# Kernel optimization log

Hardware: AMD Instinct MI355X
Metric: run time of the kernel (lower is better)

The kernel has to match this reference:

```python
import jax, jax.numpy as jnp
import numpy as np

B, T, D, H = 2, 2048, 1024, 16
HD = D // H  # head_dim = 64


def setup_inputs() -> dict:
    key = jax.random.key(0)
    ks = jax.random.split(key, 5)
    s = 0.02
    return {
        "x": jax.random.normal(ks[0], (B, T, D), dtype=jnp.float32),
        "Wqkv": jax.random.normal(ks[1], (3 * D, D), dtype=jnp.float32) * s,
        "bqkv": jax.random.normal(ks[2], (3 * D,), dtype=jnp.float32) * s,
        "Wproj": jax.random.normal(ks[3], (D, D), dtype=jnp.float32) * s,
        "bproj": jax.random.normal(ks[4], (D,), dtype=jnp.float32) * s,
    }


def reference(x, Wqkv, bqkv, Wproj, bproj):
    b, t, d = x.shape
    qkv = x @ Wqkv.T + bqkv                      # [B,T,3D]
    q, k, v = jnp.split(qkv, 3, axis=-1)
    # [B,T,D] -> [B,H,T,HD]
    def to_heads(u):
        return u.reshape(b, t, H, HD).transpose(0, 2, 1, 3)
    q, k, v = to_heads(q), to_heads(k), to_heads(v)
    scale = 1.0 / jnp.sqrt(jnp.float32(HD))
    attn = jnp.einsum("bhqd,bhkd->bhqk", q, k) * scale   # [B,H,T,T]
    causal = jnp.tril(jnp.ones((t, t), dtype=bool))
    attn = jnp.where(causal[None, None, :, :], attn, -jnp.inf)
    attn = jax.nn.softmax(attn, axis=-1)
    scores = jnp.einsum("bhqk,bhkd->bhqd", attn, v)       # [B,H,T,HD]
    scores = scores.transpose(0, 2, 1, 3).reshape(b, t, d)
    return scores @ Wproj.T + bproj
```

## Files before the change

kernel.cpp:

```cpp
#include <hip/hip_runtime.h>

typedef __bf16 bf16_8 __attribute__((ext_vector_type(8)));
typedef __bf16 bf16_4 __attribute__((ext_vector_type(4)));
typedef float  f32_4  __attribute__((ext_vector_type(4)));
typedef short  s16x4  __attribute__((ext_vector_type(4)));

typedef __attribute__((address_space(1))) const void* as1_cvp;
typedef __attribute__((address_space(3))) void*       as3_vp;

__device__ __forceinline__ void load16_to_lds(const void* g, void* l) {
    __builtin_amdgcn_global_load_lds((as1_cvp)g, (as3_vp)l, 16, 0, 0);
}

__device__ __forceinline__ f32_4 mfma16x16x16(bf16_4 a, bf16_4 b, f32_4 c) {
#if __has_builtin(__builtin_amdgcn_mfma_f32_16x16x16_bf16)
    return __builtin_amdgcn_mfma_f32_16x16x16_bf16(a, b, c, 0, 0, 0);
#else
    return __builtin_amdgcn_mfma_f32_16x16x16bf16_1k(
        __builtin_bit_cast(s16x4, a), __builtin_bit_cast(s16x4, b), c, 0, 0, 0);
#endif
}

__global__ __launch_bounds__(256) void cvt_all(
    const float* __restrict__ a, const float* __restrict__ b,
    const float* __restrict__ c, __bf16* __restrict__ out,
    int na4, int nb4, int nc4)
{
    int i = blockIdx.x * 256 + threadIdx.x;
    if (i >= na4 + nb4 + nc4) return;
    float4 f;
    if (i < na4)            f = ((const float4*)a)[i];
    else if (i < na4 + nb4) f = ((const float4*)b)[i - na4];
    else                    f = ((const float4*)c)[i - na4 - nb4];
    bf16_4 v = { (__bf16)f.x, (__bf16)f.y, (__bf16)f.z, (__bf16)f.w };
    ((bf16_4*)out)[i] = v;
}

#define BM 128

template<int OUT_BF16, int BN_>
__global__ __launch_bounds__(256) void gemm_bt(
    const __bf16* __restrict__ A,
    const __bf16* __restrict__ B,
    const float*  __restrict__ bias,
    __bf16* __restrict__ Cb, float* __restrict__ Cf,
    int M, int N, int K)
{
    constexpr int NT   = BN_ / 32;
    constexpr int CSTR = BN_ + (OUT_BF16 ? 8 : 4);
    __shared__ __align__(16) char smem[35840];
    __bf16* As = (__bf16*)smem;
    __bf16* Bs = As + 128 * 64;

    const int tid  = threadIdx.x;
    const int wave = tid >> 6;
    const int lane = tid & 63;
    const int wm = wave >> 1, wn = wave & 1;
    const int quad = lane >> 4, l16 = lane & 15;
    const int bm = blockIdx.y * BM, bn = blockIdx.x * BN_;

    const int r0 = tid >> 3;
    const int ch = tid & 7;
    const int cs = (ch ^ (r0 & 7)) * 8;

    f32_4 acc[4][NT];
    #pragma unroll
    for (int i = 0; i < 4; ++i)
        #pragma unroll
        for (int j = 0; j < NT; ++j)
            acc[i][j] = f32_4{0.f, 0.f, 0.f, 0.f};

    for (int k0 = 0; k0 < K; k0 += 64) {
        __syncthreads();
        #pragma unroll
        for (int p = 0; p < 4; ++p) {
            int row = p * 32 + r0;
            load16_to_lds(A + (size_t)(bm + row) * K + k0 + cs,
                          &As[(p * 32 + wave * 8) * 64]);
        }
        #pragma unroll
        for (int p = 0; p < BN_ / 32; ++p) {
            int row = p * 32 + r0;
            load16_to_lds(B + (size_t)(bn + row) * K + k0 + cs,
                          &Bs[(p * 32 + wave * 8) * 64]);
        }
        __syncthreads();

        #pragma unroll
        for (int h = 0; h < 2; ++h) {
            const int sl = ((quad + h * 4) ^ (l16 & 7)) * 8;
            bf16_8 af[4], bfr[NT];
            #pragma unroll
            for (int mt = 0; mt < 4; ++mt)
                af[mt] = *(const bf16_8*)&As[(wm * 64 + mt * 16 + l16) * 64 + sl];
            #pragma unroll
            for (int nt = 0; nt < NT; ++nt)
                bfr[nt] = *(const bf16_8*)&Bs[(wn * (BN_/2) + nt * 16 + l16) * 64 + sl];
            #pragma unroll
            for (int mt = 0; mt < 4; ++mt)
                #pragma unroll
                for (int nt = 0; nt < NT; ++nt)
                    acc[mt][nt] = __builtin_amdgcn_mfma_f32_16x16x32_bf16(
                        af[mt], bfr[nt], acc[mt][nt], 0, 0, 0);
        }
    }

    __syncthreads();

    if (OUT_BF16) {
        __bf16* Cs = (__bf16*)smem;
        #pragma unroll
        for (int mt = 0; mt < 4; ++mt)
            #pragma unroll
            for (int nt = 0; nt < NT; ++nt) {
                int col = wn * (BN_/2) + nt * 16 + l16;
                float bv = bias ? bias[bn + col] : 0.f;
                #pragma unroll
                for (int r = 0; r < 4; ++r)
                    Cs[(wm * 64 + mt * 16 + quad * 4 + r) * CSTR + col] =
                        (__bf16)(acc[mt][nt][r] + bv);
            }
        __syncthreads();
        const int rr = tid >> 4, cc = (tid & 15) * 8;
        #pragma unroll
        for (int p = 0; p < 8; ++p) {
            int row = p * 16 + rr;
            bf16_8 v = *(const bf16_8*)&Cs[row * CSTR + cc];
            *(bf16_8*)(Cb + (size_t)(bm + row) * N + bn + cc) = v;
        }
    } else {
        float* Cs = (float*)smem;
        #pragma unroll
        for (int mt = 0; mt < 4; ++mt)
            #pragma unroll
            for (int nt = 0; nt < NT; ++nt) {
                int col = wn * (BN_/2) + nt * 16 + l16;
                float bv = bias ? bias[bn + col] : 0.f;
                #pragma unroll
                for (int r = 0; r < 4; ++r)
                    Cs[(wm * 64 + mt * 16 + quad * 4 + r) * CSTR + col] =
                        acc[mt][nt][r] + bv;
            }
        __syncthreads();
        const int rr = tid >> 4, cc = (tid & 15) * 4;
        #pragma unroll
        for (int p = 0; p < 8; ++p) {
            int row = p * 16 + rr;
            float4 v = *(const float4*)&Cs[row * CSTR + cc];
            *(float4*)(Cf + (size_t)(bm + row) * N + bn + cc) = v;
        }
    }
}

__global__ __launch_bounds__(512, 4) void attn_kernel(
    const __bf16* __restrict__ qkv, __bf16* __restrict__ out)
{
    constexpr int T = 2048;
    __shared__ __align__(16) char pool[35328];
    __bf16* Ks = (__bf16*)pool;
    __bf16* Vt = (__bf16*)(pool + 16384);
    float*  Om = (float*)pool;
    float*  Lm = (float*)(pool + 34816);

    const int tid  = threadIdx.x;
    const int wave = tid >> 6;
    const int lane = tid & 63;
    const int wg = wave >> 2, wq = wave & 3;
    const int quad = lane >> 4, l16 = lane & 15;

    const int fid = blockIdx.x;
    const int xcd = fid & 7;
    const int w   = fid >> 3;
    const int qt  = 15 - (w >> 2);
    const int bh  = xcd * 4 + (w & 3);
    const int b = bh >> 4, h = bh & 15;
    const int jmax = 2 * qt + 1;

    const size_t rowbase = (size_t)b * T;
    const __bf16* Kbase = qkv + 1024 + h * 64;
    const __bf16* Vbase = qkv + 2048 + h * 64;

    const int krow = tid >> 3;
    const int kcbs = tid & 7;
    const int kcbf = kcbs ^ (krow & 7);
    const int vrow = krow, va = kcbs;

    bf16_8 aq[2][2];
    #pragma unroll
    for (int mt = 0; mt < 2; ++mt) {
        const __bf16* qrow =
            qkv + (rowbase + qt * 128 + wq * 32 + mt * 16 + l16) * 3072 + h * 64;
        aq[mt][0] = *(const bf16_8*)(qrow + quad * 8);
        aq[mt][1] = *(const bf16_8*)(qrow + 32 + quad * 8);
        #pragma unroll
        for (int u = 0; u < 8; ++u) {
            aq[mt][0][u] = (__bf16)((float)aq[mt][0][u] * 0.125f);
            aq[mt][1][u] = (__bf16)((float)aq[mt][1][u] * 0.125f);
        }
    }

    load16_to_lds(Kbase + (rowbase + krow) * 3072 + kcbf * 8, &Ks[wave * 512]);
    {
        bf16_8 vv = *(const bf16_8*)(Vbase + (rowbase + vrow) * 3072 + va * 8);
        int kc = vrow >> 3, kl = vrow & 7;
        #pragma unroll
        for (int u = 0; u < 8; ++u)
            Vt[(va * 8 + u) * 64 + ((kc ^ u ^ va) << 3) + kl] = vv[u];
    }

    float l_i[2] = {0.f, 0.f};
    f32_4 O[2][4];
    #pragma unroll
    for (int mt = 0; mt < 2; ++mt)
        #pragma unroll
        for (int dt = 0; dt < 4; ++dt) O[mt][dt] = f32_4{0.f, 0.f, 0.f, 0.f};

    for (int j = 0; j <= jmax; ++j) {
        const int cur = j & 1, nxt = cur ^ 1;
        __syncthreads();

        const bool stage = (j < jmax);
        bf16_8 vv;
        if (stage) {
            const int jn = j + 1;
            load16_to_lds(Kbase + (rowbase + jn * 64 + krow) * 3072 + kcbf * 8,
                          &Ks[nxt * 4096 + wave * 512]);
            vv = *(const bf16_8*)(Vbase + (rowbase + jn * 64 + vrow) * 3072 + va * 8);
        }

        f32_4 S[2][2];
        #pragma unroll
        for (int nt = 0; nt < 2; ++nt) {
            int rk = wg * 32 + nt * 16 + l16;
            int rx = rk & 7;
            bf16_8 kb0 = *(const bf16_8*)&Ks[cur * 4096 + rk * 64 + ((quad ^ rx) << 3)];
            bf16_8 kb1 = *(const bf16_8*)&Ks[cur * 4096 + rk * 64 + (((quad + 4) ^ rx) << 3)];
            #pragma unroll
            for (int mt = 0; mt < 2; ++mt) {
                f32_4 zz = {0.f, 0.f, 0.f, 0.f};
                zz = __builtin_amdgcn_mfma_f32_16x16x32_bf16(kb0, aq[mt][0], zz, 0, 0, 0);
                zz = __builtin_amdgcn_mfma_f32_16x16x32_bf16(kb1, aq[mt][1], zz, 0, 0, 0);
                S[mt][nt] = zz;
            }
        }

        const bool diag = (j >= 2 * qt);
        bf16_4 bp[2][2];
        #pragma unroll
        for (int mt = 0; mt < 2; ++mt) {
            int qg = qt * 128 + wq * 32 + mt * 16 + l16;
            #pragma unroll
            for (int nt = 0; nt < 2; ++nt) {
                #pragma unroll
                for (int rr = 0; rr < 4; ++rr) {
                    float p = __expf(S[mt][nt][rr]);
                    if (diag) {
                        int key = j * 64 + wg * 32 + nt * 16 + quad * 4 + rr;
                        if (key > qg) p = 0.f;
                    }
                    l_i[mt] += p;
                    bp[mt][nt][rr] = (__bf16)p;
                }
            }
        }

        #pragma unroll
        for (int dt = 0; dt < 4; ++dt) {
            int d = dt * 16 + l16;
            int dsw = (d & 7) ^ ((d >> 3) & 7);
            #pragma unroll
            for (int nt = 0; nt < 2; ++nt) {
                int kc16 = wg * 2 + nt;
                int chv = (kc16 * 2 + (quad >> 1)) ^ dsw;
                bf16_4 vaf = *(const bf16_4*)&Vt[cur * 4096 + d * 64 + chv * 8 + (quad & 1) * 4];
                #pragma unroll
                for (int mt = 0; mt < 2; ++mt)
                    O[mt][dt] = mfma16x16x16(vaf, bp[mt][nt], O[mt][dt]);
            }
        }

        if (stage) {
            int kc = vrow >> 3, kl = vrow & 7;
            #pragma unroll
            for (int u = 0; u < 8; ++u)
                Vt[nxt * 4096 + (va * 8 + u) * 64 + ((kc ^ u ^ va) << 3) + kl] = vv[u];
        }
    }

    float lw[2];
    #pragma unroll
    for (int mt = 0; mt < 2; ++mt) {
        float v = l_i[mt];
        v += __shfl_xor(v, 16, 64);
        v += __shfl_xor(v, 32, 64);
        lw[mt] = v;
    }
    __syncthreads();
    if (wg == 1) {
        #pragma unroll
        for (int mt = 0; mt < 2; ++mt) {
            #pragma unroll
            for (int dt = 0; dt < 4; ++dt)
                *(f32_4*)&Om[(wq * 32 + mt * 16 + l16) * 68 + dt * 16 + quad * 4] = O[mt][dt];
            if (quad == 0) Lm[wq * 32 + mt * 16 + l16] = lw[mt];
        }
    }
    __syncthreads();
    if (wg == 0) {
        #pragma unroll
        for (int mt = 0; mt < 2; ++mt) {
            float inv = 1.f / (lw[mt] + Lm[wq * 32 + mt * 16 + l16]);
            int q = qt * 128 + wq * 32 + mt * 16 + l16;
            #pragma unroll
            for (int dt = 0; dt < 4; ++dt) {
                f32_4 o2 = *(const f32_4*)&Om[(wq * 32 + mt * 16 + l16) * 68 + dt * 16 + quad * 4];
                bf16_4 ov;
                #pragma unroll
                for (int rr = 0; rr < 4; ++rr)
                    ov[rr] = (__bf16)((O[mt][dt][rr] + o2[rr]) * inv);
                *(bf16_4*)(out + (rowbase + q) * 1024 + h * 64 + dt * 16 + quad * 4) = ov;
            }
        }
    }
}

extern "C" void kernel_launch(void* const* d_in, const int* in_sizes, int n_in,
                              void* d_out, int out_size, void* d_ws, size_t ws_size,
                              hipStream_t stream)
{
    constexpr int Bc = 2, Tc = 2048, Dc = 1024;
    constexpr int M  = Bc * Tc;
    constexpr int N1 = 3 * Dc;

    const float* x     = (const float*)d_in[0];
    const float* Wqkv  = (const float*)d_in[1];
    const float* bqkv  = (const float*)d_in[2];
    const float* Wproj = (const float*)d_in[3];
    const float* bproj = (const float*)d_in[4];
    float* outp = (float*)d_out;

    __bf16* xb     = (__bf16*)d_ws;
    __bf16* wqkvb  = xb     + (size_t)M * Dc;
    __bf16* wprojb = wqkvb  + (size_t)N1 * Dc;
    __bf16* qkvb   = wprojb + (size_t)Dc * Dc;
    __bf16* attnb  = qkvb   + (size_t)M * N1;

    {
        int na4 = M * Dc / 4, nb4 = N1 * Dc / 4, nc4 = Dc * Dc / 4;
        int n4 = na4 + nb4 + nc4;
        cvt_all<<<(n4 + 255) / 256, 256, 0, stream>>>(x, Wqkv, Wproj, xb, na4, nb4, nc4);
    }

    gemm_bt<1, 128><<<dim3(N1 / 128, M / BM), 256, 0, stream>>>(
        xb, wqkvb, bqkv, qkvb, nullptr, M, N1, Dc);

    attn_kernel<<<dim3(512), 512, 0, stream>>>(qkvb, attnb);

    gemm_bt<0, 64><<<dim3(Dc / 64, M / BM), 256, 0, stream>>>(
        attnb, wprojb, bproj, nullptr, outp, M, Dc, Dc);
}
```

Baseline: 179.3 us.

## Emit V transposed from QKV GEMM epilogue and async-load it in attention

The QKV GEMM now writes Q and K into a 2048-wide buffer and writes V directly in a per-head transposed [b, d, t] layout from its epilogue. The attention kernel can then stage V tiles with async global-to-LDS loads instead of register loads followed by scalar transposing LDS stores. The work-to-block mapping is also reordered into two halves of query tiles. The cost is uncoalesced 8-byte strided stores for V in the GEMM epilogue.

After: 170.2 us. -5.0%, faster.

```diff
diff --git a/kernel.cpp b/kernel.cpp
--- a/kernel.cpp
+++ b/kernel.cpp
@@ -38,13 +38,14 @@
 
 #define BM 128
 
-template<int OUT_BF16, int BN_>
+template<int OUT_BF16, int BN_, int QKV>
 __global__ __launch_bounds__(256) void gemm_bt(
     const __bf16* __restrict__ A,
     const __bf16* __restrict__ B,
     const float*  __restrict__ bias,
     __bf16* __restrict__ Cb, float* __restrict__ Cf,
-    int M, int N, int K)
+    __bf16* __restrict__ Vtb,
+    int M, int N, int K, int ldc)
 {
     constexpr int NT   = BN_ / 32;
     constexpr int CSTR = BN_ + (OUT_BF16 ? 8 : 4);
@@ -105,6 +106,26 @@
         }
     }
 
+    if (QKV && bn >= 2048) {
+        const int b_ = bm >> 11;
+        const int t0 = (bm & 2047) + wm * 64;
+        #pragma unroll
+        for (int nt = 0; nt < NT; ++nt) {
+            int vrow = (bn - 2048) + wn * (BN_/2) + nt * 16 + l16;
+            float bv = bias ? bias[2048 + vrow] : 0.f;
+            #pragma unroll
+            for (int mt = 0; mt < 4; ++mt) {
+                bf16_4 ov;
+                #pragma unroll
+                for (int r = 0; r < 4; ++r)
+                    ov[r] = (__bf16)(acc[mt][nt][r] + bv);
+                *(bf16_4*)(Vtb + ((size_t)b_ * 1024 + vrow) * 2048
+                           + t0 + mt * 16 + quad * 4) = ov;
+            }
+        }
+        return;
+    }
+
     __syncthreads();
 
     if (OUT_BF16) {
@@ -126,7 +147,7 @@
         for (int p = 0; p < 8; ++p) {
             int row = p * 16 + rr;
             bf16_8 v = *(const bf16_8*)&Cs[row * CSTR + cc];
-            *(bf16_8*)(Cb + (size_t)(bm + row) * N + bn + cc) = v;
+            *(bf16_8*)(Cb + (size_t)(bm + row) * ldc + bn + cc) = v;
         }
     } else {
         float* Cs = (float*)smem;
@@ -147,13 +168,14 @@
         for (int p = 0; p < 8; ++p) {
             int row = p * 16 + rr;
             float4 v = *(const float4*)&Cs[row * CSTR + cc];
-            *(float4*)(Cf + (size_t)(bm + row) * N + bn + cc) = v;
+            *(float4*)(Cf + (size_t)(bm + row) * ldc + bn + cc) = v;
         }
     }
 }
 
 __global__ __launch_bounds__(512, 4) void attn_kernel(
-    const __bf16* __restrict__ qkv, __bf16* __restrict__ out)
+    const __bf16* __restrict__ qk, const __bf16* __restrict__ vt,
+    __bf16* __restrict__ out)
 {
     constexpr int T = 2048;
     __shared__ __align__(16) char pool[35328];
@@ -168,28 +190,28 @@
     const int wg = wave >> 2, wq = wave & 3;
     const int quad = lane >> 4, l16 = lane & 15;
 
-    const int fid = blockIdx.x;
-    const int xcd = fid & 7;
-    const int w   = fid >> 3;
-    const int qt  = 15 - (w >> 2);
-    const int bh  = xcd * 4 + (w & 3);
+    const int fid  = blockIdx.x;
+    const int xcd  = fid & 7;
+    const int half = fid >> 8;
+    const int w    = (fid >> 3) & 31;
+    const int qt   = half ? (7 - (w >> 2)) : ((w >> 2) + 8);
+    const int bh   = xcd * 4 + (w & 3);
     const int b = bh >> 4, h = bh & 15;
     const int jmax = 2 * qt + 1;
 
     const size_t rowbase = (size_t)b * T;
-    const __bf16* Kbase = qkv + 1024 + h * 64;
-    const __bf16* Vbase = qkv + 2048 + h * 64;
-
-    const int krow = tid >> 3;
-    const int kcbs = tid & 7;
-    const int kcbf = kcbs ^ (krow & 7);
-    const int vrow = krow, va = kcbs;
+    const __bf16* Kbase = qk + 1024 + h * 64;
+    const __bf16* Vbase = vt + (size_t)bh * 64 * 2048;
+
+    const int srow = tid >> 3;
+    const int sch  = tid & 7;
+    const int schf = sch ^ (srow & 7);
 
     bf16_8 aq[2][2];
     #pragma unroll
     for (int mt = 0; mt < 2; ++mt) {
         const __bf16* qrow =
-            qkv + (rowbase + qt * 128 + wq * 32 + mt * 16 + l16) * 3072 + h * 64;
+            qk + (rowbase + qt * 128 + wq * 32 + mt * 16 + l16) * 2048 + h * 64;
         aq[mt][0] = *(const bf16_8*)(qrow + quad * 8);
         aq[mt][1] = *(const bf16_8*)(qrow + 32 + quad * 8);
         #pragma unroll
@@ -199,14 +221,8 @@
         }
     }
 
-    load16_to_lds(Kbase + (rowbase + krow) * 3072 + kcbf * 8, &Ks[wave * 512]);
-    {
-        bf16_8 vv = *(const bf16_8*)(Vbase + (rowbase + vrow) * 3072 + va * 8);
-        int kc = vrow >> 3, kl = vrow & 7;
-        #pragma unroll
-        for (int u = 0; u < 8; ++u)
-            Vt[(va * 8 + u) * 64 + ((kc ^ u ^ va) << 3) + kl] = vv[u];
-    }
+    load16_to_lds(Kbase + (rowbase + srow) * 2048 + schf * 8, &Ks[wave * 512]);
+    load16_to_lds(Vbase + (size_t)srow * 2048 + schf * 8,     &Vt[wave * 512]);
 
     float l_i[2] = {0.f, 0.f};
     f32_4 O[2][4];
@@ -219,13 +235,12 @@
         const int cur = j & 1, nxt = cur ^ 1;
         __syncthreads();
 
-        const bool stage = (j < jmax);
-        bf16_8 vv;
-        if (stage) {
+        if (j < jmax) {
             const int jn = j + 1;
-            load16_to_lds(Kbase + (rowbase + jn * 64 + krow) * 3072 + kcbf * 8,
+            load16_to_lds(Kbase + (rowbase + jn * 64 + srow) * 2048 + schf * 8,
                           &Ks[nxt * 4096 + wave * 512]);
-            vv = *(const bf16_8*)(Vbase + (rowbase + jn * 64 + vrow) * 3072 + va * 8);
+            load16_to_lds(Vbase + (size_t)srow * 2048 + jn * 64 + schf * 8,
+                          &Vt[nxt * 4096 + wave * 512]);
         }
 
         f32_4 S[2][2];
@@ -267,23 +282,15 @@
         #pragma unroll
         for (int dt = 0; dt < 4; ++dt) {
             int d = dt * 16 + l16;
-            int dsw = (d & 7) ^ ((d >> 3) & 7);
+            int dsw = d & 7;
             #pragma unroll
             for (int nt = 0; nt < 2; ++nt) {
-                int kc16 = wg * 2 + nt;
-                int chv = (kc16 * 2 + (quad >> 1)) ^ dsw;
+                int chv = (wg * 4 + nt * 2 + (quad >> 1)) ^ dsw;
                 bf16_4 vaf = *(const bf16_4*)&Vt[cur * 4096 + d * 64 + chv * 8 + (quad & 1) * 4];
                 #pragma unroll
                 for (int mt = 0; mt < 2; ++mt)
                     O[mt][dt] = mfma16x16x16(vaf, bp[mt][nt], O[mt][dt]);
             }
-        }
-
-        if (stage) {
-            int kc = vrow >> 3, kl = vrow & 7;
-            #pragma unroll
-            for (int u = 0; u < 8; ++u)
-                Vt[nxt * 4096 + (va * 8 + u) * 64 + ((kc ^ u ^ va) << 3) + kl] = vv[u];
         }
     }
 
@@ -342,8 +349,9 @@
     __bf16* xb     = (__bf16*)d_ws;
     __bf16* wqkvb  = xb     + (size_t)M * Dc;
     __bf16* wprojb = wqkvb  + (size_t)N1 * Dc;
-    __bf16* qkvb   = wprojb + (size_t)Dc * Dc;
-    __bf16* attnb  = qkvb   + (size_t)M * N1;
+    __bf16* qkb    = wprojb + (size_t)Dc * Dc;
+    __bf16* vtb    = qkb    + (size_t)M * 2048;
+    __bf16* attnb  = vtb    + (size_t)Bc * 1024 * 2048;
 
     {
         int na4 = M * Dc / 4, nb4 = N1 * Dc / 4, nc4 = Dc * Dc / 4;
@@ -351,11 +359,11 @@
         cvt_all<<<(n4 + 255) / 256, 256, 0, stream>>>(x, Wqkv, Wproj, xb, na4, nb4, nc4);
     }
 
-    gemm_bt<1, 128><<<dim3(N1 / 128, M / BM), 256, 0, stream>>>(
-        xb, wqkvb, bqkv, qkvb, nullptr, M, N1, Dc);
-
-    attn_kernel<<<dim3(512), 512, 0, stream>>>(qkvb, attnb);
-
-    gemm_bt<0, 64><<<dim3(Dc / 64, M / BM), 256, 0, stream>>>(
-        attnb, wprojb, bproj, nullptr, outp, M, Dc, Dc);
-}
+    gemm_bt<1, 128, 1><<<dim3(N1 / 128, M / BM), 256, 0, stream>>>(
+        xb, wqkvb, bqkv, qkb, nullptr, vtb, M, N1, Dc, 2048);
+
+    attn_kernel<<<dim3(512), 512, 0, stream>>>(qkb, vtb, attnb);
+
+    gemm_bt<0, 64, 0><<<dim3(Dc / 64, M / BM), 256, 0, stream>>>(
+        attnb, wprojb, bproj, nullptr, outp, nullptr, M, Dc, Dc, Dc);
+}
```
